# Kernel tuning notes

Measured on AMD Instinct MI355X. Metric: run time of the kernel, lower is better.

## Reference

```python
import jax, jax.numpy as jnp
import numpy as np

B, OBS, L, D, BINS, HID = 4096, 128, 4, 8, 16, 512
S = L * D  # max_seq_len = 32; qchunk_size = S, single Q chunk


def _lin(k, i, o, s):
    kw, kb = jax.random.split(k)
    return jax.random.normal(kw, (i, o), jnp.float32) * s, jnp.zeros((o,), jnp.float32)


def setup_inputs() -> dict:
    key = jax.random.key(0)
    ks = jax.random.split(key, 12)
    inp = {
        "obs": jax.random.normal(ks[0], (B, OBS), jnp.float32),
        "category": jax.random.randint(ks[1], (B, L, D), 0, BINS, jnp.int32),
    }
    # v_network: obs_dim -> 512 -> 512 -> 512 -> 1 (tanh hidden)
    dims_v = [OBS, HID, HID, HID, 1]
    for i in range(4):
        w, b = _lin(ks[2 + i], dims_v[i], dims_v[i + 1], 0.05)
        inp[f"v_w{i}"], inp[f"v_b{i}"] = w, b
    # q_network: (obs_dim+actor_dim) -> 512 -> 512 -> 512 -> bins*S
    dims_q = [OBS + D, HID, HID, HID, BINS * S]
    for i in range(4):
        w, b = _lin(ks[6 + i], dims_q[i], dims_q[i + 1], 0.05)
        inp[f"q_w{i}"], inp[f"q_b{i}"] = w, b
    return inp


def _mlp(x, ws, bs):
    for w, b in zip(ws[:-1], bs[:-1]):
        x = jnp.tanh(x @ w + b)
    return x @ ws[-1] + bs[-1]


def _actions_from_category(category):
    # zoom_in per (level, dim): width_l = 2/bins^(l+1); low accumulates cat*width.
    cat = category.astype(jnp.float32)  # (B, L, D)
    widths = 2.0 / (jnp.float32(BINS) ** jnp.arange(1, L + 1, dtype=jnp.float32))  # (L,)
    cum_low = jnp.cumsum(cat * widths[None, :, None], axis=1)  # (B, L, D)
    mids = -1.0 + cum_low + 0.5 * widths[None, :, None]  # midpoint after each level
    # mids_full[:, j, d] = midpoint of dim d after j zoom-in updates (j=0 -> 0.0)
    mids_full = jnp.concatenate(
        [jnp.zeros((category.shape[0], 1, D), jnp.float32), mids], axis=1)  # (B, L+1, D)
    # at sequence step k (input to Q), dim d' has had U[k,d'] updates
    k = jnp.arange(S)
    U = k[:, None] // D + (jnp.arange(D)[None, :] < (k[:, None] % D)).astype(jnp.int32)  # (S, D)
    dgrid = jnp.broadcast_to(jnp.arange(D)[None, :], (S, D))
    return mids_full[:, U, dgrid]  # (B, S, D)


def reference(obs, category,
              v_w0, v_b0, v_w1, v_b1, v_w2, v_b2, v_w3, v_b3,
              q_w0, q_b0, q_w1, q_b1, q_w2, q_b2, q_w3, q_b3):
    vw = [v_w0, v_w1, v_w2, v_w3]; vb = [v_b0, v_b1, v_b2, v_b3]
    qw = [q_w0, q_w1, q_w2, q_w3]; qb = [q_b0, q_b1, q_b2, q_b3]
    b = obs.shape[0]
    actions = _actions_from_category(category)  # (B, S, D)
    obs_rep = jnp.broadcast_to(obs[:, None, :], (b, S, OBS))
    x = jnp.concatenate([obs_rep, actions], axis=-1)  # (B, S, OBS+D)
    adv = _mlp(x, qw, qb)  # (B, S, S*BINS)
    adv = adv.reshape(b, S, S, BINS)
    s_idx = jnp.arange(S)
    adv = adv[:, s_idx, s_idx, :]  # diagonal gather -> (B, S, BINS)
    adv = adv.reshape(b, L, D, BINS)
    value = _mlp(obs, vw, vb)  # (B, 1)
    nbias = jnp.zeros((b, L, D, 1), jnp.float32)  # use_nbias=False
    return value, adv, nbias
```

## Files before the change

kernel.cpp:

```cpp
#include <hip/hip_runtime.h>
#include <hip/hip_bf16.h>

#define B_SZ   4096
#define OBS_N  128
#define HID    512
#define TANH_SCALE 2.885390081777927f


typedef __bf16 bf16x8_t __attribute__((ext_vector_type(8)));
typedef float  f32x4_t  __attribute__((ext_vector_type(4)));

__device__ inline float fast_tanh(float x) {
    float e = __builtin_amdgcn_exp2f(x * TANH_SCALE);
    return fmaf(-2.f, __builtin_amdgcn_rcpf(e + 1.f), 1.f);
}

__device__ inline float fast_tanh_pre(float x) {
    float e = __builtin_amdgcn_exp2f(x);
    return fmaf(-2.f, __builtin_amdgcn_rcpf(e + 1.f), 1.f);
}

__device__ inline void gld_lds16(const void* g, void* l) {
    __builtin_amdgcn_global_load_lds(
        (const __attribute__((address_space(1))) void*)g,
        (__attribute__((address_space(3))) void*)l, 16, 0, 0);
}

__device__ inline int hs_off(int row, int col) {
    int c = col >> 3;
    int phys = (c & ~7) | ((c ^ (row & 7)) & 7);
    return row * 512 + phys * 8 + (col & 7);
}

__global__ __launch_bounds__(256) void prep_kernel(
    const float* __restrict__ obs, const int* __restrict__ category,
    const float* __restrict__ qw0, const float* __restrict__ qb0,
    const float* __restrict__ qw1, const float* __restrict__ qw2,
    const float* __restrict__ qw3,
    const float* __restrict__ vw0, const float* __restrict__ vb0,
    const float* __restrict__ vw1, const float* __restrict__ vw2,
    const float* __restrict__ qb1, const float* __restrict__ qb2,
    const float* __restrict__ vb1, const float* __restrict__ vb2,
    __hip_bfloat16* __restrict__ obs_bf,
    __hip_bfloat16* __restrict__ w0t, __hip_bfloat16* __restrict__ w1t,
    __hip_bfloat16* __restrict__ w2t, __hip_bfloat16* __restrict__ w3t,
    __hip_bfloat16* __restrict__ vw0t, __hip_bfloat16* __restrict__ vw1t,
    __hip_bfloat16* __restrict__ vw2t,
    __hip_bfloat16* __restrict__ w0aug, __hip_bfloat16* __restrict__ vw0aug,
    __hip_bfloat16* __restrict__ acts_bf, float* __restrict__ bias_s,
    float* __restrict__ nbias)
{
    const int bid = blockIdx.x, tid = threadIdx.x;
    if (bid < 2048) {
        int i = bid * 256 + tid;
        obs_bf[i] = __float2bfloat16(obs[i]);
    } else if (bid < 2560) {
        const float* src = (bid < 2304) ? qw0 : vw0;
        __hip_bfloat16* dst = (bid < 2304) ? w0t : vw0t;
        int idx = ((bid - 2048) & 255) * 256 + tid;
        int n = idx >> 7, k = idx & 127;
        dst[idx] = __float2bfloat16(src[k * 512 + n] * TANH_SCALE);
    } else if (bid < 7680) {
        int job = (bid - 2560) >> 10;
        const float* srcs[5] = {qw1, qw2, qw3, vw1, vw2};
        __hip_bfloat16* dsts[5] = {w1t, w2t, w3t, vw1t, vw2t};
        float sc = (job == 2) ? 1.0f : TANH_SCALE;
        int idx = ((bid - 2560) & 1023) * 256 + tid;
        int e    = idx & 7;
        int lane = (idx >> 3) & 63;
        int kc   = (idx >> 9) & 15;
        int tile = idx >> 13;
        int k = kc * 32 + (lane >> 4) * 8 + e;
        int n = tile * 16 + (lane & 15);
        dsts[job][idx] = __float2bfloat16(srcs[job][k * 512 + n] * sc);
    } else if (bid < 11776) {
        int t = (bid - 7680) * 256 + tid;
        int d = t & 7;
        int r = t >> 3;
        int b = r & 4095, s = r >> 12;
        int U = (s >> 3) + ((d < (s & 7)) ? 1 : 0);
        float a = 0.f;
        if (U > 0) {
            float w = 0.125f, cum = 0.f;
            for (int j = 0; j < U; ++j) {
                cum += (float)category[b * 32 + j * 8 + d] * w;
                if (j == U - 1) a = -1.f + cum + 0.5f * w;
                w *= 0.0625f;
            }
        }
        acts_bf[t] = __float2bfloat16(a);
    } else if (bid < 11904) {
        int sub = bid - 11776;
        bool isv = sub >= 64;
        int idx = (sub & 63) * 256 + tid;
        int e    = idx & 7;
        int lane = (idx >> 3) & 63;
        int tile = idx >> 9;
        int k = (lane >> 4) * 8 + e;
        int n = tile * 16 + (lane & 15);
        float v = 0.f;
        if (!isv) {
            if (k < 8) v = qw0[(128 + k) * 512 + n];
            else if (k == 8) v = qb0[n];
            w0aug[idx] = __float2bfloat16(v * TANH_SCALE);
        } else {
            if (k == 8) v = vb0[n];
            vw0aug[idx] = __float2bfloat16(v * TANH_SCALE);
        }
    } else if (bid < 11912) {
        int idx = (bid - 11904) * 256 + tid;
        const float* srcs[4] = {qb1, qb2, vb1, vb2};
        bias_s[idx] = srcs[idx >> 9][idx & 511] * TANH_SCALE;
    } else {
        int i = (bid - 11912) * 256 + tid;
        nbias[i] = 0.f;
    }
}

__global__ __launch_bounds__(256) void gemm_dual(
    const __hip_bfloat16* __restrict__ A0, const __hip_bfloat16* __restrict__ B0,
    const float* __restrict__ bias0, void* __restrict__ C0, int K0, int epi0, int nb0,
    const __hip_bfloat16* __restrict__ A1, const __hip_bfloat16* __restrict__ B1,
    const float* __restrict__ bias1, void* __restrict__ C1, int K1, int epi1)
{
    __shared__ __hip_bfloat16 As[128 * 32];
    __shared__ __hip_bfloat16 Bs[128 * 32];

    const __hip_bfloat16 *A, *Bt;
    const float* bias;
    void* Cout;
    int K, epi, tb;
    if ((int)blockIdx.x < nb0) {
        A = A0; Bt = B0; bias = bias0; Cout = C0; K = K0; epi = epi0; tb = blockIdx.x;
    } else {
        A = A1; Bt = B1; bias = bias1; Cout = C1; K = K1; epi = epi1; tb = blockIdx.x - nb0;
    }
    const long m0 = (long)(tb >> 2) * 128;
    const int  n0 = (tb & 3) * 128;

    const int tid  = threadIdx.x;
    const int wave = tid >> 6, lane = tid & 63;
    const int quad = lane >> 4, t = lane & 15;
    const int wr = wave >> 1, wc = wave & 1;

    f32x4_t acc[4][4] = {};

    const int lrow  = lane >> 2;
    const int lkoff = (((lane & 3) + (lane >> 3)) & 3) * 8;

    const __hip_bfloat16* Ag0 = A  + (m0 + wave * 32 +      lrow) * (long)K + lkoff;
    const __hip_bfloat16* Ag1 = A  + (m0 + wave * 32 + 16 + lrow) * (long)K + lkoff;
    const __hip_bfloat16* Bg0 = Bt + (long)(n0 + wave * 32 +      lrow) * K + lkoff;
    const __hip_bfloat16* Bg1 = Bt + (long)(n0 + wave * 32 + 16 + lrow) * K + lkoff;
    __hip_bfloat16* AsB0 = &As[(wave * 32) * 32];
    __hip_bfloat16* AsB1 = &As[(wave * 32 + 16) * 32];
    __hip_bfloat16* BsB0 = &Bs[(wave * 32) * 32];
    __hip_bfloat16* BsB1 = &Bs[(wave * 32 + 16) * 32];

    const int slot = ((quad - (t >> 1)) & 3) * 8;

    for (int k0 = 0; k0 < K; k0 += 32) {
        gld_lds16(Ag0 + k0, AsB0);
        gld_lds16(Ag1 + k0, AsB1);
        gld_lds16(Bg0 + k0, BsB0);
        gld_lds16(Bg1 + k0, BsB1);
        __syncthreads();
        bf16x8_t af[4], bfr[4];
        #pragma unroll
        for (int i = 0; i < 4; ++i)
            af[i] = *(const bf16x8_t*)&As[(wr * 64 + i * 16 + t) * 32 + slot];
        #pragma unroll
        for (int j = 0; j < 4; ++j)
            bfr[j] = *(const bf16x8_t*)&Bs[(wc * 64 + j * 16 + t) * 32 + slot];
        #pragma unroll
        for (int i = 0; i < 4; ++i)
            #pragma unroll
            for (int j = 0; j < 4; ++j)
                acc[i][j] = __builtin_amdgcn_mfma_f32_16x16x32_bf16(af[i], bfr[j], acc[i][j], 0, 0, 0);
        __syncthreads();
    }

    #pragma unroll
    for (int i = 0; i < 4; ++i) {
        const long rbase = m0 + wr * 64 + i * 16 + quad * 4;
        #pragma unroll
        for (int j = 0; j < 4; ++j) {
            const int col = n0 + wc * 64 + j * 16 + t;
            #pragma unroll
            for (int r = 0; r < 4; ++r) {
                float v = acc[i][j][r];
                if (epi == 1) {
                    v = fast_tanh(v + bias[col]);
                    ((__hip_bfloat16*)Cout)[(rbase + r) * 512 + col] = __float2bfloat16(v);
                } else if (epi == 2) {
                    ((__hip_bfloat16*)Cout)[(rbase + r) * 512 + col] = __float2bfloat16(v);
                } else if (epi == 3) {
                    const long m = rbase + r;
                    const int brow = (int)(m & 63);
                    const long idx =
                        ((((m >> 6) * 8 + (col >> 6)) * 16 + (brow >> 4) * 4 + ((col >> 4) & 3)) * 256)
                        + ((col >> 2) & 3) * 64 + (brow & 15) * 4 + (col & 3);
                    ((float*)Cout)[idx] = v;
                } else {
                    ((float*)Cout)[(rbase + r) * 512 + col] = v;
                }
            }
        }
    }
}

__device__ inline void epi_store(
    __hip_bfloat16* hs, f32x4_t acc[4][4],
    int n0w, int quad, int t)
{
    #pragma unroll
    for (int j = 0; j < 4; ++j) {
        const int oc0 = n0w + j * 16 + quad * 4;
        const int cbase = oc0 >> 3;
        const int sub = (quad & 1) * 4;
        #pragma unroll
        for (int rt = 0; rt < 4; ++rt) {
            const int row = rt * 16 + t;
            union { __hip_bfloat16 b[4]; uint2 v; } o;
            o.b[0] = __float2bfloat16(fast_tanh_pre(acc[rt][j][0]));
            o.b[1] = __float2bfloat16(fast_tanh_pre(acc[rt][j][1]));
            o.b[2] = __float2bfloat16(fast_tanh_pre(acc[rt][j][2]));
            o.b[3] = __float2bfloat16(fast_tanh_pre(acc[rt][j][3]));
            const int phys = (cbase & ~7) | ((cbase ^ (row & 7)) & 7);
            *(uint2*)&hs[row * 512 + phys * 8 + sub] = o.v;
        }
    }
}

__device__ inline void mfma_layer(
    __hip_bfloat16* hs, const __hip_bfloat16* __restrict__ Wt,
    const float* __restrict__ bias_s, int w, int lane)
{
    const int quad = lane >> 4, t = lane & 15;
    const int n0w = w * 64;
    const __hip_bfloat16* Wl = Wt + ((size_t)(w * 4) * 16 * 64 + lane) * 8;
    f32x4_t acc[4][4];
    #pragma unroll
    for (int j = 0; j < 4; ++j) {
        const f32x4_t bv = *(const f32x4_t*)&bias_s[n0w + j * 16 + quad * 4];
        #pragma unroll
        for (int rt = 0; rt < 4; ++rt)
            acc[rt][j] = bv;
    }
    bf16x8_t wc[4], wn[4], ac[4];
    #pragma unroll
    for (int j = 0; j < 4; ++j)
        wc[j] = *(const bf16x8_t*)(Wl + (size_t)(j * 16) * 512);

    #pragma unroll 2
    for (int kc = 0; kc < 16; ++kc) {
        const int craw = kc * 4 + quad;
        const int phys = (craw & ~7) | ((craw ^ (t & 7)) & 7);
        #pragma unroll
        for (int rt = 0; rt < 4; ++rt)
            ac[rt] = *(const bf16x8_t*)&hs[(rt * 16 + t) * 512 + phys * 8];
        if (kc < 15) {
            #pragma unroll
            for (int j = 0; j < 4; ++j)
                wn[j] = *(const bf16x8_t*)(Wl + (size_t)(j * 16 + kc + 1) * 512);
        }
        __builtin_amdgcn_s_setprio(1);
        #pragma unroll
        for (int j = 0; j < 4; ++j)
            #pragma unroll
            for (int rt = 0; rt < 4; ++rt)
                acc[rt][j] = __builtin_amdgcn_mfma_f32_16x16x32_bf16(wc[j], ac[rt], acc[rt][j], 0, 0, 0);
        __builtin_amdgcn_s_setprio(0);
        #pragma unroll
        for (int j = 0; j < 4; ++j) wc[j] = wn[j];
    }
    __syncthreads();
    epi_store(hs, acc, n0w, quad, t);
    __syncthreads();
}

__global__ __launch_bounds__(512, 4) void fused_kernel(
    const float* __restrict__ p,
    const float* __restrict__ pv,
    const __hip_bfloat16* __restrict__ acts_bf,
    const __hip_bfloat16* __restrict__ w0aug,
    const __hip_bfloat16* __restrict__ vw0aug,
    const __hip_bfloat16* __restrict__ w1t, const float* __restrict__ qb1s,
    const __hip_bfloat16* __restrict__ w2t, const float* __restrict__ qb2s,
    const __hip_bfloat16* __restrict__ w3t, const float* __restrict__ qb3,
    float* __restrict__ advout,
    const __hip_bfloat16* __restrict__ vw1t, const float* __restrict__ vb1s,
    const __hip_bfloat16* __restrict__ vw2t, const float* __restrict__ vb2s,
    const float* __restrict__ vw3, const float* __restrict__ vb3,
    float* __restrict__ vout)
{
    __shared__ __hip_bfloat16 hs[64 * 512];
    const int bid = blockIdx.x;
    const int tid = threadIdx.x;
    const int w = tid >> 6, lane = tid & 63;
    const int quad = lane >> 4, t = lane & 15;
    const bool is_q = bid < 2048;
    const int s  = is_q ? (bid >> 6) : 0;
    const int mb = is_q ? (bid & 63) : (bid - 2048);
    const int n0w = w * 64;

    {
        const float* Pt = (is_q ? p : pv) + (((size_t)mb * 8 + w) * 16) * 256 + lane * 4;
        const __hip_bfloat16* W0 = is_q ? w0aug : vw0aug;
        f32x4_t acc[4][4];
        #pragma unroll
        for (int rt = 0; rt < 4; ++rt)
            #pragma unroll
            for (int j = 0; j < 4; ++j)
                acc[rt][j] = *(const f32x4_t*)(Pt + (rt * 4 + j) * 256);
        bf16x8_t bfrag[4];
        #pragma unroll
        for (int rt = 0; rt < 4; ++rt) {
            union { bf16x8_t vec; unsigned short u[8]; } bu;
            #pragma unroll
            for (int i = 0; i < 8; ++i) bu.u[i] = 0;
            if (quad == 1) bu.u[0] = 0x3F80;
            if (is_q && quad == 0) {
                const long r = (long)s * 4096 + mb * 64 + rt * 16 + t;
                bu.vec = *(const bf16x8_t*)&acts_bf[r * 8];
            }
            bfrag[rt] = bu.vec;
        }
        bf16x8_t wq[4];
        #pragma unroll
        for (int j = 0; j < 4; ++j)
            wq[j] = *(const bf16x8_t*)(W0 + ((size_t)(w * 4 + j) * 64 + lane) * 8);
        __builtin_amdgcn_s_setprio(1);
        #pragma unroll
        for (int j = 0; j < 4; ++j)
            #pragma unroll
            for (int rt = 0; rt < 4; ++rt)
                acc[rt][j] = __builtin_amdgcn_mfma_f32_16x16x32_bf16(wq[j], bfrag[rt], acc[rt][j], 0, 0, 0);
        __builtin_amdgcn_s_setprio(0);
        epi_store(hs, acc, n0w, quad, t);
    }
    __syncthreads();

    mfma_layer(hs, is_q ? w1t : vw1t, is_q ? qb1s : vb1s, w, lane);
    mfma_layer(hs, is_q ? w2t : vw2t, is_q ? qb2s : vb2s, w, lane);

    if (is_q) {
        f32x4_t acc = {};
        if (w < 4) {
            const __hip_bfloat16* W3l = w3t + ((size_t)s * 16 * 64 + (size_t)lane) * 8;
            #pragma unroll 4
            for (int kc = 0; kc < 16; ++kc) {
                const int craw = kc * 4 + quad;
                const int phys = (craw & ~7) | ((craw ^ (t & 7)) & 7);
                bf16x8_t a = *(const bf16x8_t*)&hs[(w * 16 + t) * 512 + phys * 8];
                bf16x8_t bq = *(const bf16x8_t*)(W3l + (size_t)kc * 512);
                acc = __builtin_amdgcn_mfma_f32_16x16x32_bf16(a, bq, acc, 0, 0, 0);
            }
        }
        __syncthreads();
        float* hsf = (float*)hs;
        if (w < 4) {
            const float bias3 = qb3[s * 16 + t];
            #pragma unroll
            for (int rr = 0; rr < 4; ++rr)
                hsf[(w * 16 + quad * 4 + rr) * 16 + t] = acc[rr] + bias3;
        }
        __syncthreads();
        const int row = tid >> 3, cp = tid & 7;
        float2 v2 = *(const float2*)&hsf[row * 16 + cp * 2];
        *(float2*)&advout[(size_t)(mb * 64 + row) * 512 + s * 16 + cp * 2] = v2;
    } else {
        const int row = tid >> 3, seg = tid & 7;
        float sum = 0.f;
        for (int k = seg * 64; k < seg * 64 + 64; ++k)
            sum += __bfloat162float(hs[hs_off(row, k)]) * vw3[k];
        sum += __shfl_xor(sum, 1);
        sum += __shfl_xor(sum, 2);
        sum += __shfl_xor(sum, 4);
        if (seg == 0) vout[mb * 64 + row] = sum + vb3[0];
    }
}

extern "C" void kernel_launch(void* const* d_in, const int* in_sizes, int n_in,
                              void* d_out, int out_size, void* d_ws, size_t ws_size,
                              hipStream_t stream) {
    const float* obs      = (const float*)d_in[0];
    const int*   category = (const int*)d_in[1];
    const float* v_w0 = (const float*)d_in[2];
    const float* v_b0 = (const float*)d_in[3];
    const float* v_w1 = (const float*)d_in[4];
    const float* v_b1 = (const float*)d_in[5];
    const float* v_w2 = (const float*)d_in[6];
    const float* v_b2 = (const float*)d_in[7];
    const float* v_w3 = (const float*)d_in[8];
    const float* v_b3 = (const float*)d_in[9];
    const float* q_w0 = (const float*)d_in[10];
    const float* q_b0 = (const float*)d_in[11];
    const float* q_w1 = (const float*)d_in[12];
    const float* q_b1 = (const float*)d_in[13];
    const float* q_w2 = (const float*)d_in[14];
    const float* q_b2 = (const float*)d_in[15];
    const float* q_w3 = (const float*)d_in[16];
    const float* q_b3 = (const float*)d_in[17];

    char* ws = (char*)d_ws;
    __hip_bfloat16* obs_bf = (__hip_bfloat16*)(ws + 0);
    __hip_bfloat16* w0t    = (__hip_bfloat16*)(ws + 1048576);
    __hip_bfloat16* vw0t   = (__hip_bfloat16*)(ws + 1179648);
    __hip_bfloat16* w1t    = (__hip_bfloat16*)(ws + 1310720);
    __hip_bfloat16* w2t    = (__hip_bfloat16*)(ws + 1835008);
    __hip_bfloat16* w3t    = (__hip_bfloat16*)(ws + 2359296);
    __hip_bfloat16* vw1t   = (__hip_bfloat16*)(ws + 2883584);
    __hip_bfloat16* vw2t   = (__hip_bfloat16*)(ws + 3407872);
    __hip_bfloat16* w0aug  = (__hip_bfloat16*)(ws + 3932160);
    __hip_bfloat16* vw0aug = (__hip_bfloat16*)(ws + 3964928);
    __hip_bfloat16* acts_bf= (__hip_bfloat16*)(ws + 3997696);
    float*          p      = (float*)         (ws + 6094848);
    float*          pv     = (float*)         (ws + 14483456);
    float*          bias_s = (float*)         (ws + 22872064);

    float* out       = (float*)d_out;
    float* out_value = out;
    float* out_adv   = out + 4096;
    float* out_nbias = out + 4096 + (size_t)B_SZ * 512;

    prep_kernel<<<12424, 256, 0, stream>>>(
        obs, category, q_w0, q_b0, q_w1, q_w2, q_w3, v_w0, v_b0, v_w1, v_w2,
        q_b1, q_b2, v_b1, v_b2,
        obs_bf, w0t, w1t, w2t, w3t, vw0t, vw1t, vw2t, w0aug, vw0aug,
        acts_bf, bias_s, out_nbias);

    gemm_dual<<<256, 256, 0, stream>>>(
        obs_bf, w0t, nullptr, p, 128, 3, 128,
        obs_bf, vw0t, nullptr, pv, 128, 3);

    fused_kernel<<<2112, 512, 0, stream>>>(
        p, pv, acts_bf, w0aug, vw0aug,
        w1t, bias_s, w2t, bias_s + 512, w3t, q_b3, out_adv,
        vw1t, bias_s + 1024, vw2t, bias_s + 1536, v_w3, v_b3, out_value);
}
```

Measured before the change: 262.8 us.

## Split row tile into halves and overlap tanh epilogue with MFMA of other half

Splits each 64-row hidden layer into two 32-row halves, so the tanh/bf16 epilogue stores of one half are interleaved into the MFMA k-loop of the other half, which reads disjoint LDS rows. The hidden-layer weights are re-laid out so the four 16-column tiles for each k-chunk are contiguous, and the register prefetch of the next chunk is dropped in favour of full unrolling. The aim is to hide the epilogue's transcendental and LDS store cost behind matrix work. In exchange, each layer's weights are now streamed twice per block, and there are extra barriers between phases.

```diff
diff --git a/kernel.cpp b/kernel.cpp
--- a/kernel.cpp
+++ b/kernel.cpp
@@ -68,8 +68,16 @@
         int idx = ((bid - 2560) & 1023) * 256 + tid;
         int e    = idx & 7;
         int lane = (idx >> 3) & 63;
-        int kc   = (idx >> 9) & 15;
-        int tile = idx >> 13;
+        int tile, kc;
+        if (job == 2) {
+            kc   = (idx >> 9) & 15;
+            tile = idx >> 13;
+        } else {
+            int jj = (idx >> 9) & 3;
+            kc     = (idx >> 11) & 15;
+            int g  = idx >> 15;
+            tile = g * 4 + jj;
+        }
         int k = kc * 32 + (lane >> 4) * 8 + e;
         int n = tile * 16 + (lane & 15);
         dsts[job][idx] = __float2bfloat16(srcs[job][k * 512 + n] * sc);
@@ -209,74 +217,85 @@
     }
 }
 
-__device__ inline void epi_store(
-    __hip_bfloat16* hs, f32x4_t acc[4][4],
-    int n0w, int quad, int t)
-{
-    #pragma unroll
-    for (int j = 0; j < 4; ++j) {
-        const int oc0 = n0w + j * 16 + quad * 4;
-        const int cbase = oc0 >> 3;
-        const int sub = (quad & 1) * 4;
-        #pragma unroll
-        for (int rt = 0; rt < 4; ++rt) {
-            const int row = rt * 16 + t;
-            union { __hip_bfloat16 b[4]; uint2 v; } o;
-            o.b[0] = __float2bfloat16(fast_tanh_pre(acc[rt][j][0]));
-            o.b[1] = __float2bfloat16(fast_tanh_pre(acc[rt][j][1]));
-            o.b[2] = __float2bfloat16(fast_tanh_pre(acc[rt][j][2]));
-            o.b[3] = __float2bfloat16(fast_tanh_pre(acc[rt][j][3]));
-            const int phys = (cbase & ~7) | ((cbase ^ (row & 7)) & 7);
-            *(uint2*)&hs[row * 512 + phys * 8 + sub] = o.v;
-        }
-    }
-}
-
-__device__ inline void mfma_layer(
+__device__ inline void epi_group(
+    __hip_bfloat16* hs, const f32x4_t a, int row, int oc0, int sub)
+{
+    const int cbase = oc0 >> 3;
+    union { __hip_bfloat16 b[4]; uint2 v; } o;
+    o.b[0] = __float2bfloat16(fast_tanh_pre(a[0]));
+    o.b[1] = __float2bfloat16(fast_tanh_pre(a[1]));
+    o.b[2] = __float2bfloat16(fast_tanh_pre(a[2]));
+    o.b[3] = __float2bfloat16(fast_tanh_pre(a[3]));
+    const int phys = (cbase & ~7) | ((cbase ^ (row & 7)) & 7);
+    *(uint2*)&hs[row * 512 + phys * 8 + sub] = o.v;
+}
+
+template<int HM, int HE, bool DO_EPI>
+__device__ inline void layer_phase(
     __hip_bfloat16* hs, const __hip_bfloat16* __restrict__ Wt,
-    const float* __restrict__ bias_s, int w, int lane)
+    const float* __restrict__ bias_s,
+    f32x4_t (&accC)[2][4], f32x4_t (&accP)[2][4],
+    int w, int lane)
 {
     const int quad = lane >> 4, t = lane & 15;
     const int n0w = w * 64;
-    const __hip_bfloat16* Wl = Wt + ((size_t)(w * 4) * 16 * 64 + lane) * 8;
-    f32x4_t acc[4][4];
+    const int sub = (quad & 1) * 4;
+    const __hip_bfloat16* Wl = Wt + (size_t)w * 32768 + (size_t)lane * 8;
     #pragma unroll
     for (int j = 0; j < 4; ++j) {
         const f32x4_t bv = *(const f32x4_t*)&bias_s[n0w + j * 16 + quad * 4];
-        #pragma unroll
-        for (int rt = 0; rt < 4; ++rt)
-            acc[rt][j] = bv;
-    }
-    bf16x8_t wc[4], wn[4], ac[4];
-    #pragma unroll
-    for (int j = 0; j < 4; ++j)
-        wc[j] = *(const bf16x8_t*)(Wl + (size_t)(j * 16) * 512);
-
-    #pragma unroll 2
+        accC[0][j] = bv;
+        accC[1][j] = bv;
+    }
+    #pragma unroll
     for (int kc = 0; kc < 16; ++kc) {
         const int craw = kc * 4 + quad;
         const int phys = (craw & ~7) | ((craw ^ (t & 7)) & 7);
-        #pragma unroll
-        for (int rt = 0; rt < 4; ++rt)
-            ac[rt] = *(const bf16x8_t*)&hs[(rt * 16 + t) * 512 + phys * 8];
-        if (kc < 15) {
-            #pragma unroll
-            for (int j = 0; j < 4; ++j)
-                wn[j] = *(const bf16x8_t*)(Wl + (size_t)(j * 16 + kc + 1) * 512);
-        }
+        bf16x8_t a0 = *(const bf16x8_t*)&hs[(HM * 32 + t) * 512 + phys * 8];
+        bf16x8_t a1 = *(const bf16x8_t*)&hs[(HM * 32 + 16 + t) * 512 + phys * 8];
+        bf16x8_t wv[4];
+        #pragma unroll
+        for (int j = 0; j < 4; ++j)
+            wv[j] = *(const bf16x8_t*)(Wl + (size_t)(kc * 4 + j) * 512);
         __builtin_amdgcn_s_setprio(1);
         #pragma unroll
+        for (int j = 0; j < 4; ++j) {
+            accC[0][j] = __builtin_amdgcn_mfma_f32_16x16x32_bf16(wv[j], a0, accC[0][j], 0, 0, 0);
+            accC[1][j] = __builtin_amdgcn_mfma_f32_16x16x32_bf16(wv[j], a1, accC[1][j], 0, 0, 0);
+        }
+        __builtin_amdgcn_s_setprio(0);
+        if (DO_EPI && kc < 8) {
+            const int j = kc & 3, rt = kc >> 2;
+            epi_group(hs, accP[rt][j], HE * 32 + rt * 16 + t,
+                      n0w + j * 16 + quad * 4, sub);
+        }
+    }
+}
+
+template<int H>
+__device__ inline void phase0_half(
+    const float* __restrict__ Pt, const __hip_bfloat16* __restrict__ acts_bf,
+    bool is_q, long rglob, const bf16x8_t (&wq)[4],
+    f32x4_t (&acc)[2][4], int quad, int t)
+{
+    #pragma unroll
+    for (int rt = 0; rt < 2; ++rt)
+        #pragma unroll
         for (int j = 0; j < 4; ++j)
-            #pragma unroll
-            for (int rt = 0; rt < 4; ++rt)
-                acc[rt][j] = __builtin_amdgcn_mfma_f32_16x16x32_bf16(wc[j], ac[rt], acc[rt][j], 0, 0, 0);
-        __builtin_amdgcn_s_setprio(0);
-        #pragma unroll
-        for (int j = 0; j < 4; ++j) wc[j] = wn[j];
-    }
-    __syncthreads();
-    epi_store(hs, acc, n0w, quad, t);
-    __syncthreads();
+            acc[rt][j] = *(const f32x4_t*)(Pt + ((H * 2 + rt) * 4 + j) * 256);
+    #pragma unroll
+    for (int rt = 0; rt < 2; ++rt) {
+        union { bf16x8_t vec; unsigned short u[8]; } bu;
+        #pragma unroll
+        for (int i = 0; i < 8; ++i) bu.u[i] = 0;
+        if (quad == 1) bu.u[0] = 0x3F80;
+        if (is_q && quad == 0)
+            bu.vec = *(const bf16x8_t*)&acts_bf[(rglob + (H * 2 + rt) * 16 + t) * 8];
+        bf16x8_t bfr = bu.vec;
+        #pragma unroll
+        for (int j = 0; j < 4; ++j)
+            acc[rt][j] = __builtin_amdgcn_mfma_f32_16x16x32_bf16(wq[j], bfr, acc[rt][j], 0, 0, 0);
+    }
 }
 
 __global__ __launch_bounds__(512, 4) void fused_kernel(
@@ -299,50 +318,51 @@
     const int tid = threadIdx.x;
     const int w = tid >> 6, lane = tid & 63;
     const int quad = lane >> 4, t = lane & 15;
+    const int sub = (quad & 1) * 4;
     const bool is_q = bid < 2048;
     const int s  = is_q ? (bid >> 6) : 0;
     const int mb = is_q ? (bid & 63) : (bid - 2048);
     const int n0w = w * 64;
 
+    const __hip_bfloat16* Wt1 = is_q ? w1t : vw1t;
+    const __hip_bfloat16* Wt2 = is_q ? w2t : vw2t;
+    const float* b1 = is_q ? qb1s : vb1s;
+    const float* b2 = is_q ? qb2s : vb2s;
+
+    f32x4_t accA[2][4], accB[2][4];
+
     {
         const float* Pt = (is_q ? p : pv) + (((size_t)mb * 8 + w) * 16) * 256 + lane * 4;
         const __hip_bfloat16* W0 = is_q ? w0aug : vw0aug;
-        f32x4_t acc[4][4];
-        #pragma unroll
-        for (int rt = 0; rt < 4; ++rt)
-            #pragma unroll
-            for (int j = 0; j < 4; ++j)
-                acc[rt][j] = *(const f32x4_t*)(Pt + (rt * 4 + j) * 256);
-        bf16x8_t bfrag[4];
-        #pragma unroll
-        for (int rt = 0; rt < 4; ++rt) {
-            union { bf16x8_t vec; unsigned short u[8]; } bu;
-            #pragma unroll
-            for (int i = 0; i < 8; ++i) bu.u[i] = 0;
-            if (quad == 1) bu.u[0] = 0x3F80;
-            if (is_q && quad == 0) {
-                const long r = (long)s * 4096 + mb * 64 + rt * 16 + t;
-                bu.vec = *(const bf16x8_t*)&acts_bf[r * 8];
-            }
-            bfrag[rt] = bu.vec;
-        }
+        const long rglob = (long)s * 4096 + mb * 64;
         bf16x8_t wq[4];
         #pragma unroll
         for (int j = 0; j < 4; ++j)
             wq[j] = *(const bf16x8_t*)(W0 + ((size_t)(w * 4 + j) * 64 + lane) * 8);
-        __builtin_amdgcn_s_setprio(1);
-        #pragma unroll
-        for (int j = 0; j < 4; ++j)
-            #pragma unroll
-            for (int rt = 0; rt < 4; ++rt)
-                acc[rt][j] = __builtin_amdgcn_mfma_f32_16x16x32_bf16(wq[j], bfrag[rt], acc[rt][j], 0, 0, 0);
-        __builtin_amdgcn_s_setprio(0);
-        epi_store(hs, acc, n0w, quad, t);
-    }
-    __syncthreads();
-
-    mfma_layer(hs, is_q ? w1t : vw1t, is_q ? qb1s : vb1s, w, lane);
-    mfma_layer(hs, is_q ? w2t : vw2t, is_q ? qb2s : vb2s, w, lane);
+        phase0_half<0>(Pt, acts_bf, is_q, rglob, wq, accA, quad, t);
+        phase0_half<1>(Pt, acts_bf, is_q, rglob, wq, accB, quad, t);
+        #pragma unroll
+        for (int g = 0; g < 8; ++g) {
+            const int j = g & 3, rt = g >> 2;
+            epi_group(hs, accA[rt][j], rt * 16 + t, n0w + j * 16 + quad * 4, sub);
+        }
+    }
+    __syncthreads();
+
+    layer_phase<0, 1, true>(hs, Wt1, b1, accA, accB, w, lane);
+    __syncthreads();
+    layer_phase<1, 0, true>(hs, Wt1, b1, accB, accA, w, lane);
+    __syncthreads();
+    layer_phase<0, 1, true>(hs, Wt2, b2, accA, accB, w, lane);
+    __syncthreads();
+    layer_phase<1, 0, true>(hs, Wt2, b2, accB, accA, w, lane);
+    __syncthreads();
+    #pragma unroll
+    for (int g = 0; g < 8; ++g) {
+        const int j = g & 3, rt = g >> 2;
+        epi_group(hs, accB[rt][j], 32 + rt * 16 + t, n0w + j * 16 + quad * 4, sub);
+    }
+    __syncthreads();
 
     if (is_q) {
         f32x4_t acc = {};
```

Measured after the change: 325.4 us. +23.8%, slower.

## Reorder packed weight layout per warp and double-buffer weight fragments across k-chunks

Applied to the files above, without the earlier changes.

Packs the hidden-layer weights (except the final q layer) so that each warp's four 16-column tiles for a given k-chunk sit contiguously, making each warp's weight stream one linear 64 KB region. The MFMA loop now keeps two register sets of weight fragments, ping-ponged across even and odd k-chunks, so the global loads for chunk k+2 are issued right after chunk k's MFMAs. The aim is to improve global access locality and hide weight load latency. The cost is higher register pressure under the 4-waves launch bound.

```diff
diff --git a/kernel.cpp b/kernel.cpp
--- a/kernel.cpp
+++ b/kernel.cpp
@@ -68,8 +68,16 @@
         int idx = ((bid - 2560) & 1023) * 256 + tid;
         int e    = idx & 7;
         int lane = (idx >> 3) & 63;
-        int kc   = (idx >> 9) & 15;
-        int tile = idx >> 13;
+        int tile, kc;
+        if (job == 2) {
+            kc   = (idx >> 9) & 15;
+            tile = idx >> 13;
+        } else {
+            int jj = (idx >> 9) & 3;
+            kc     = (idx >> 11) & 15;
+            int g  = idx >> 15;
+            tile = g * 4 + jj;
+        }
         int k = kc * 32 + (lane >> 4) * 8 + e;
         int n = tile * 16 + (lane & 15);
         dsts[job][idx] = __float2bfloat16(srcs[job][k * 512 + n] * sc);
@@ -238,7 +246,7 @@
 {
     const int quad = lane >> 4, t = lane & 15;
     const int n0w = w * 64;
-    const __hip_bfloat16* Wl = Wt + ((size_t)(w * 4) * 16 * 64 + lane) * 8;
+    const __hip_bfloat16* Wl = Wt + (size_t)w * 32768 + (size_t)lane * 8;
     f32x4_t acc[4][4];
     #pragma unroll
     for (int j = 0; j < 4; ++j) {
@@ -247,32 +255,54 @@
         for (int rt = 0; rt < 4; ++rt)
             acc[rt][j] = bv;
     }
-    bf16x8_t wc[4], wn[4], ac[4];
+    bf16x8_t wA[4], wB[4], ac[4];
     #pragma unroll
-    for (int j = 0; j < 4; ++j)
-        wc[j] = *(const bf16x8_t*)(Wl + (size_t)(j * 16) * 512);
-
-    #pragma unroll 2
-    for (int kc = 0; kc < 16; ++kc) {
-        const int craw = kc * 4 + quad;
-        const int phys = (craw & ~7) | ((craw ^ (t & 7)) & 7);
-        #pragma unroll
-        for (int rt = 0; rt < 4; ++rt)
-            ac[rt] = *(const bf16x8_t*)&hs[(rt * 16 + t) * 512 + phys * 8];
-        if (kc < 15) {
+    for (int j = 0; j < 4; ++j) {
+        wA[j] = *(const bf16x8_t*)(Wl + (size_t)(0 * 4 + j) * 512);
+        wB[j] = *(const bf16x8_t*)(Wl + (size_t)(1 * 4 + j) * 512);
+    }
+
+    for (int m = 0; m < 8; ++m) {
+        {
+            const int kc = 2 * m;
+            const int craw = kc * 4 + quad;
+            const int phys = (craw & ~7) | ((craw ^ (t & 7)) & 7);
+            #pragma unroll
+            for (int rt = 0; rt < 4; ++rt)
+                ac[rt] = *(const bf16x8_t*)&hs[(rt * 16 + t) * 512 + phys * 8];
+            __builtin_amdgcn_s_setprio(1);
             #pragma unroll
             for (int j = 0; j < 4; ++j)
-                wn[j] = *(const bf16x8_t*)(Wl + (size_t)(j * 16 + kc + 1) * 512);
-        }
-        __builtin_amdgcn_s_setprio(1);
-        #pragma unroll
-        for (int j = 0; j < 4; ++j)
+                #pragma unroll
+                for (int rt = 0; rt < 4; ++rt)
+                    acc[rt][j] = __builtin_amdgcn_mfma_f32_16x16x32_bf16(wA[j], ac[rt], acc[rt][j], 0, 0, 0);
+            __builtin_amdgcn_s_setprio(0);
+            if (m < 7) {
+                #pragma unroll
+                for (int j = 0; j < 4; ++j)
+                    wA[j] = *(const bf16x8_t*)(Wl + (size_t)((kc + 2) * 4 + j) * 512);
+            }
+        }
+        {
+            const int kc = 2 * m + 1;
+            const int craw = kc * 4 + quad;
+            const int phys = (craw & ~7) | ((craw ^ (t & 7)) & 7);
             #pragma unroll
             for (int rt = 0; rt < 4; ++rt)
-                acc[rt][j] = __builtin_amdgcn_mfma_f32_16x16x32_bf16(wc[j], ac[rt], acc[rt][j], 0, 0, 0);
-        __builtin_amdgcn_s_setprio(0);
-        #pragma unroll
-        for (int j = 0; j < 4; ++j) wc[j] = wn[j];
+                ac[rt] = *(const bf16x8_t*)&hs[(rt * 16 + t) * 512 + phys * 8];
+            __builtin_amdgcn_s_setprio(1);
+            #pragma unroll
+            for (int j = 0; j < 4; ++j)
+                #pragma unroll
+                for (int rt = 0; rt < 4; ++rt)
+                    acc[rt][j] = __builtin_amdgcn_mfma_f32_16x16x32_bf16(wB[j], ac[rt], acc[rt][j], 0, 0, 0);
+            __builtin_amdgcn_s_setprio(0);
+            if (m < 7) {
+                #pragma unroll
+                for (int j = 0; j < 4; ++j)
+                    wB[j] = *(const bf16x8_t*)(Wl + (size_t)((kc + 2) * 4 + j) * 512);
+            }
+        }
     }
     __syncthreads();
     epi_store(hs, acc, n0w, quad, t);
```

After: 255.9 us. 1.03x faster.
